# Kernel optimization log

Measured on AMD Instinct MI355X. Metric: run time of the kernel, lower is better.

## Reference

```python
import jax, jax.numpy as jnp
import numpy as np

N_NODES = 10000
N_EDGES = 100000
IN_CH = 384
PROJ = 768  # in_channels * projection_factor
N_BLOCKS = 4
OUT_CH = 128
LN_EPS = 1e-5


def _p(key, shape, fan_in):
    return jax.random.normal(key, shape, dtype=jnp.float32) * (1.0 / np.sqrt(fan_in))


def setup_inputs() -> dict:
    key = jax.random.key(0)
    ks = iter(jax.random.split(key, 64))
    x = jax.random.normal(next(ks), (N_NODES, IN_CH), dtype=jnp.float32)
    edge_index = jax.random.randint(next(ks), (2, N_EDGES), 0, N_NODES, dtype=jnp.int64)
    inp = {
        'x': x,
        'edge_index': edge_index,
        'proj_W': _p(next(ks), (PROJ, IN_CH), IN_CH),
        'proj_b': jnp.zeros((PROJ,), jnp.float32),
        'norm_w': jnp.ones((N_BLOCKS, PROJ), jnp.float32),
        'norm_b': jnp.zeros((N_BLOCKS, PROJ), jnp.float32),
        'g1_W': _p(next(ks), (N_BLOCKS, 4 * 192, PROJ), PROJ),
        'g1_as': _p(next(ks), (N_BLOCKS, 4, 192), 192),
        'g1_ad': _p(next(ks), (N_BLOCKS, 4, 192), 192),
        'g1_b': jnp.zeros((N_BLOCKS, 4 * 192), jnp.float32),
        'g2_W': _p(next(ks), (N_BLOCKS, 2 * 96, PROJ), PROJ),
        'g2_as': _p(next(ks), (N_BLOCKS, 2, 96), 96),
        'g2_ad': _p(next(ks), (N_BLOCKS, 2, 96), 96),
        'g2_b': jnp.zeros((N_BLOCKS, 2 * 96), jnp.float32),
        'uni_W': _p(next(ks), (N_BLOCKS, PROJ, 960), 960),
        'uni_b': jnp.zeros((N_BLOCKS, PROJ), jnp.float32),
        'fnorm_w': jnp.ones((PROJ,), jnp.float32),
        'fnorm_b': jnp.zeros((PROJ,), jnp.float32),
        'fg_W': _p(next(ks), (8 * OUT_CH, PROJ), PROJ),
        'fg_as': _p(next(ks), (8, OUT_CH), OUT_CH),
        'fg_ad': _p(next(ks), (8, OUT_CH), OUT_CH),
        'fg_b': jnp.zeros((OUT_CH,), jnp.float32),
    }
    return inp


def layer_norm(x, w, b):
    m = x.mean(-1, keepdims=True)
    v = ((x - m) ** 2).mean(-1, keepdims=True)
    return (x - m) / jnp.sqrt(v + LN_EPS) * w + b


def gat_conv(x, src, dst, W, a_src, a_dst, bias, heads, out_ch, concat):
    # PyG GATConv (eval mode, add_self_loops already applied in src/dst).
    n = x.shape[0]
    h = (x @ W.T).reshape(n, heads, out_ch)          # [N,H,C]
    al_s = jnp.einsum('nhc,hc->nh', h, a_src)        # [N,H]
    al_d = jnp.einsum('nhc,hc->nh', h, a_dst)
    e = jax.nn.leaky_relu(al_s[src] + al_d[dst], 0.2)  # [E,H]
    emax = jax.ops.segment_max(e, dst, num_segments=n)
    ee = jnp.exp(e - emax[dst])
    den = jax.ops.segment_sum(ee, dst, num_segments=n)
    alpha = ee / (den[dst] + 1e-16)                  # softmax over incoming edges
    out = jax.ops.segment_sum(h[src] * alpha[:, :, None], dst, num_segments=n)
    out = out.reshape(n, heads * out_ch) if concat else out.mean(axis=1)
    return out + bias


def reference(x, edge_index, proj_W, proj_b, norm_w, norm_b,
              g1_W, g1_as, g1_ad, g1_b, g2_W, g2_as, g2_ad, g2_b,
              uni_W, uni_b, fnorm_w, fnorm_b, fg_W, fg_as, fg_ad, fg_b):
    n = x.shape[0]
    loop = jnp.arange(n, dtype=edge_index.dtype)
    src = jnp.concatenate([edge_index[0], loop])  # add self loops (PyG default)
    dst = jnp.concatenate([edge_index[1], loop])

    h = jax.nn.elu(x @ proj_W.T + proj_b)
    for i in range(N_BLOCKS):
        res = h
        hn = layer_norm(h, norm_w[i], norm_b[i])
        o1 = gat_conv(hn, src, dst, g1_W[i], g1_as[i], g1_ad[i], g1_b[i], 4, 192, True)
        o2 = gat_conv(hn, src, dst, g2_W[i], g2_as[i], g2_ad[i], g2_b[i], 2, 96, True)
        cat = jax.nn.elu(jnp.concatenate([o1, o2], axis=-1))  # [N,960]
        h = jax.nn.elu(res + cat @ uni_W[i].T + uni_b[i])
    h = layer_norm(h, fnorm_w, fnorm_b)
    return gat_conv(h, src, dst, fg_W, fg_as, fg_ad, fg_b, 8, OUT_CH, False)
```

## Files before the change

kernel.cpp:

```cpp
#include <hip/hip_runtime.h>
#include <math.h>

#define N_NODES 10000
#define N_EDGES 100000
#define E_TOT   (N_EDGES + N_NODES)
#define PROJ    768
#define LN_EPS  1e-5f

typedef __attribute__((ext_vector_type(8))) short bf16x8;
typedef __attribute__((ext_vector_type(4))) short bf16x4;
typedef __attribute__((ext_vector_type(4))) float f32x4;

__device__ __forceinline__ float elu_f(float x){ return x > 0.f ? x : __expf(x) - 1.f; }
__device__ __forceinline__ float bf2f(unsigned short u){ return __uint_as_float(((unsigned int)u) << 16); }
__device__ __forceinline__ unsigned short f2bf(float f){
  unsigned int u = __float_as_uint(f);
  return (unsigned short)((u + 0x7FFFu + ((u >> 16) & 1u)) >> 16);
}

#define GLOAD16(gp, lp) __builtin_amdgcn_global_load_lds((const __attribute__((address_space(1))) void*)(gp), (__attribute__((address_space(3))) void*)(lp), 16, 0, 0)

__global__ void k_count(const int* __restrict__ ei, int* __restrict__ cnt){
  int e = blockIdx.x*blockDim.x + threadIdx.x;
  if (e >= E_TOT) return;
  int dst = (e < N_EDGES) ? ei[N_EDGES + e] : (e - N_EDGES);
  atomicAdd(&cnt[dst], 1);
}

__global__ void k_scan(const int* __restrict__ cnt, int* __restrict__ indptr, int* __restrict__ pos){
  __shared__ int s[1024];
  __shared__ int s_running;
  int t = threadIdx.x;
  if (t == 0) s_running = 0;
  __syncthreads();
  for (int base = 0; base < N_NODES; base += 1024){
    int v = (base + t < N_NODES) ? cnt[base + t] : 0;
    s[t] = v; __syncthreads();
    for (int off = 1; off < 1024; off <<= 1){
      int add = (t >= off) ? s[t - off] : 0;
      __syncthreads();
      s[t] += add;
      __syncthreads();
    }
    int total = s[1023];
    int run = s_running;
    if (base + t < N_NODES){
      int val = run + s[t] - v;
      indptr[base + t] = val;
      pos[base + t] = val;
    }
    __syncthreads();
    if (t == 0) s_running = run + total;
    __syncthreads();
  }
  if (t == 0) indptr[N_NODES] = s_running;
}

__global__ void k_fill(const int* __restrict__ ei, int* __restrict__ pos,
                       int* __restrict__ csr_src){
  int e = blockIdx.x*blockDim.x + threadIdx.x;
  if (e >= E_TOT) return;
  int s, d;
  if (e < N_EDGES){ s = ei[e]; d = ei[N_EDGES + e]; }
  else            { s = d = e - N_EDGES; }
  int p = atomicAdd(&pos[d], 1);
  csr_src[p] = s;
}

__global__ void k_f2bf_arr4(const float4* __restrict__ in, ushort4* __restrict__ out, int n4){
  int i = blockIdx.x*blockDim.x + threadIdx.x;
  if (i < n4){
    float4 v = in[i];
    ushort4 o;
    o.x = f2bf(v.x); o.y = f2bf(v.y); o.z = f2bf(v.z); o.w = f2bf(v.w);
    out[i] = o;
  }
}

__global__ void k_pack_l1l2(const float* __restrict__ g1, const float* __restrict__ g2,
                            unsigned short* __restrict__ dst){
  int i = blockIdx.x*blockDim.x + threadIdx.x;
  if (i >= 737280) return;
  int layer = i / 184320;
  int off4  = i - layer*184320;
  float4 v;
  if (off4 < 147456) v = *((const float4*)(g1 + (size_t)layer*589824) + off4);
  else               v = *((const float4*)(g2 + (size_t)layer*147456) + (off4 - 147456));
  ushort4 o;
  o.x = f2bf(v.x); o.y = f2bf(v.y); o.z = f2bf(v.z); o.w = f2bf(v.w);
  ((ushort4*)(dst + (size_t)layer*737280))[off4] = o;
}

__global__ void k_layernorm_bf(const unsigned short* __restrict__ x, const float* __restrict__ w,
                               const float* __restrict__ b, unsigned short* __restrict__ y){
  int n = blockIdx.x;
  int t = threadIdx.x;
  const unsigned short* xr = x + (size_t)n*PROJ;
  float v0=0.f, v1=0.f, v2=0.f, v3=0.f;
  if (t < 192){
    bf16x4 hv = *(const bf16x4*)(xr + t*4);
    v0 = bf2f((unsigned short)hv.x); v1 = bf2f((unsigned short)hv.y);
    v2 = bf2f((unsigned short)hv.z); v3 = bf2f((unsigned short)hv.w);
  }
  float s  = v0+v1+v2+v3;
  float s2 = v0*v0 + v1*v1 + v2*v2 + v3*v3;
  #pragma unroll
  for (int off = 32; off; off >>= 1){ s += __shfl_down(s, off); s2 += __shfl_down(s2, off); }
  __shared__ float rs[4], rs2[4];
  __shared__ float s_mean, s_rstd;
  int wid = t >> 6, lane = t & 63;
  if (lane == 0){ rs[wid] = s; rs2[wid] = s2; }
  __syncthreads();
  if (t == 0){
    float S  = rs[0]+rs[1]+rs[2]+rs[3];
    float S2 = rs2[0]+rs2[1]+rs2[2]+rs2[3];
    float m  = S * (1.f/768.f);
    float var = S2 * (1.f/768.f) - m*m;
    s_mean = m; s_rstd = rsqrtf(var + LN_EPS);
  }
  __syncthreads();
  if (t < 192){
    float m = s_mean, r = s_rstd;
    float4 wv = *(const float4*)&w[t*4];
    float4 bv = *(const float4*)&b[t*4];
    ushort4 o;
    o.x = f2bf((v0-m)*r*wv.x + bv.x);
    o.y = f2bf((v1-m)*r*wv.y + bv.y);
    o.z = f2bf((v2-m)*r*wv.z + bv.z);
    o.w = f2bf((v3-m)*r*wv.w + bv.w);
    *(ushort4*)(y + (size_t)n*PROJ + t*4) = o;
  }
}

template<int EPI>
__global__ __launch_bounds__(256, 8)
void k_gemm_mfma(const unsigned short* __restrict__ A, int lda,
                 const unsigned short* __restrict__ W,
                 unsigned short* __restrict__ C, int ldc,
                 int M, int N, int K,
                 const float* __restrict__ bias,
                 const unsigned short* __restrict__ res, int ldres, int NBN){
  __shared__ unsigned short As[2][128*32];
  __shared__ unsigned short Bs[2][64*32];
  const int tid = threadIdx.x;
  const int lane = tid & 63, wid = tid >> 6;
  const int wm = wid >> 1, wn = wid & 1;

  const int nwg = gridDim.x;
  const int q = nwg >> 3, r = nwg & 7;
  const int xcd = blockIdx.x & 7, o = blockIdx.x >> 3;
  const int swz = (xcd < r ? xcd*(q+1) : r*(q+1) + (xcd - r)*q) + o;
  const int bm = (swz / NBN) * 128;
  const int bn = (swz % NBN) * 64;

  const int srow = tid >> 2;
  const int sc   = (tid & 3) ^ ((tid >> 3) & 3);
  size_t ga0 = (size_t)min(bm + srow,      M-1)*lda + sc*8;
  size_t ga1 = (size_t)min(bm + 64 + srow, M-1)*lda + sc*8;
  size_t gb0 = (size_t)min(bn + srow,      N-1)*K   + sc*8;
  const int ldst = tid*8;

  f32x4 acc[4][2];
  #pragma unroll
  for (int i=0;i<4;i++)
    #pragma unroll
    for (int j=0;j<2;j++) acc[i][j] = (f32x4){0.f,0.f,0.f,0.f};

  const int rA = wm*64 + (lane & 15);
  const int rB = wn*32 + (lane & 15);
  const int cu = (((lane >> 4)) ^ (((lane & 15) >> 1) & 3)) * 8;

  const int NT = K >> 5;
  int cur = 0;
  GLOAD16(A + ga0, &As[0][ldst]);
  GLOAD16(A + ga1, &As[0][2048 + ldst]);
  GLOAD16(W + gb0, &Bs[0][ldst]);

  for (int t = 0; t < NT; ++t){
    if (t + 1 < NT){
      const int k0 = (t+1) << 5;
      GLOAD16(A + ga0 + k0, &As[cur^1][ldst]);
      GLOAD16(A + ga1 + k0, &As[cur^1][2048 + ldst]);
      GLOAD16(W + gb0 + k0, &Bs[cur^1][ldst]);
      asm volatile("s_waitcnt vmcnt(3)" ::: "memory");
    } else {
      asm volatile("s_waitcnt vmcnt(0)" ::: "memory");
    }
    __builtin_amdgcn_sched_barrier(0);
    __builtin_amdgcn_s_barrier();
    __builtin_amdgcn_sched_barrier(0);

    bf16x8 af[4], bfr[2];
    #pragma unroll
    for (int mi = 0; mi < 4; mi++)
      af[mi] = *(const bf16x8*)&As[cur][(rA + mi*16)*32 + cu];
    #pragma unroll
    for (int ni = 0; ni < 2; ni++)
      bfr[ni] = *(const bf16x8*)&Bs[cur][(rB + ni*16)*32 + cu];
    #pragma unroll
    for (int mi = 0; mi < 4; mi++)
      #pragma unroll
      for (int ni = 0; ni < 2; ni++)
        acc[mi][ni] = __builtin_amdgcn_mfma_f32_16x16x32_bf16(af[mi], bfr[ni], acc[mi][ni], 0,0,0);

    asm volatile("s_waitcnt lgkmcnt(0)" ::: "memory");
    __builtin_amdgcn_sched_barrier(0);
    __builtin_amdgcn_s_barrier();
    __builtin_amdgcn_sched_barrier(0);
    cur ^= 1;
  }

  const int mrow0 = bm + wm*64 + ((lane>>4)<<2);
  const int ncol0 = bn + wn*32 + (lane & 15);
  #pragma unroll
  for (int mi=0; mi<4; mi++){
    #pragma unroll
    for (int rr=0; rr<4; rr++){
      int m = mrow0 + mi*16 + rr;
      if (m >= M) continue;
      #pragma unroll
      for (int ni=0; ni<2; ni++){
        int n = ncol0 + ni*16;
        float v = acc[mi][ni][rr];
        if (EPI == 1){
          v = elu_f(v + bias[n]);
        } else if (EPI == 2){
          v = elu_f(v + bias[n] + bf2f(res[(size_t)m*ldres + n]));
        }
        C[(size_t)m*ldc + n] = f2bf(v);
      }
    }
  }
}

__global__ void k_attn_coef6(const unsigned short* __restrict__ hlin,
                             const float* __restrict__ as1, const float* __restrict__ ad1,
                             const float* __restrict__ as2, const float* __restrict__ ad2,
                             float* __restrict__ als, float* __restrict__ ald){
  int n = blockIdx.x;
  int wid = threadIdx.x >> 6, lane = threadIdx.x & 63;
  int C    = wid < 4 ? 192 : 96;
  int base = wid < 4 ? wid*192 : 768 + (wid-4)*96;
  const float* as_ = wid < 4 ? as1 + wid*192 : as2 + (wid-4)*96;
  const float* ad_ = wid < 4 ? ad1 + wid*192 : ad2 + (wid-4)*96;
  float ss = 0.f, sd = 0.f;
  if (lane*4 < C){
    bf16x4 hv = *(const bf16x4*)(hlin + (size_t)n*960 + base + lane*4);
    float4 a1 = *(const float4*)&as_[lane*4];
    float4 a2 = *(const float4*)&ad_[lane*4];
    float h0 = bf2f((unsigned short)hv.x), h1 = bf2f((unsigned short)hv.y);
    float h2 = bf2f((unsigned short)hv.z), h3 = bf2f((unsigned short)hv.w);
    ss = h0*a1.x + h1*a1.y + h2*a1.z + h3*a1.w;
    sd = h0*a2.x + h1*a2.y + h2*a2.z + h3*a2.w;
  }
  #pragma unroll
  for (int off = 32; off; off >>= 1){ ss += __shfl_down(ss, off); sd += __shfl_down(sd, off); }
  if (lane == 0){ als[n*6 + wid] = ss; ald[n*6 + wid] = sd; }
}

__global__ void k_attn_coef8(const unsigned short* __restrict__ hlin,
                             const float* __restrict__ a_src, const float* __restrict__ a_dst,
                             float* __restrict__ als, float* __restrict__ ald){
  int n = blockIdx.x;
  int wid = threadIdx.x >> 6, lane = threadIdx.x & 63;
  float ss = 0.f, sd = 0.f;
  if (lane < 32){
    bf16x4 hv = *(const bf16x4*)(hlin + (size_t)n*1024 + wid*128 + lane*4);
    float4 a1 = *(const float4*)&a_src[wid*128 + lane*4];
    float4 a2 = *(const float4*)&a_dst[wid*128 + lane*4];
    float h0 = bf2f((unsigned short)hv.x), h1 = bf2f((unsigned short)hv.y);
    float h2 = bf2f((unsigned short)hv.z), h3 = bf2f((unsigned short)hv.w);
    ss = h0*a1.x + h1*a1.y + h2*a1.z + h3*a1.w;
    sd = h0*a2.x + h1*a2.y + h2*a2.z + h3*a2.w;
  }
  #pragma unroll
  for (int off = 32; off; off >>= 1){ ss += __shfl_down(ss, off); sd += __shfl_down(sd, off); }
  if (lane == 0){ als[n*8 + wid] = ss; ald[n*8 + wid] = sd; }
}

template<int MODE>
__global__ __launch_bounds__(256)
void k_attn_fused(const unsigned short* __restrict__ hlin, int ldh,
                  const float* __restrict__ als, const float* __restrict__ ald,
                  const int* __restrict__ indptr, const int* __restrict__ csr_src,
                  const float* __restrict__ b1, const float* __restrict__ b2,
                  void* __restrict__ outv, int ldo){
  constexpr int TOT = MODE ? 1024 : 960;
  constexpr int HT  = MODE ? 8 : 6;
  constexpr int CH8 = TOT/8;
  constexpr int CPL = (CH8 + 63)/64;
  int n = blockIdx.x;
  int tid = threadIdx.x;
  int wv = tid >> 6, lane = tid & 63;
  int beg = indptr[n], end = indptr[n+1], deg = end - beg;

  __shared__ float s_m[HT], s_dinv[HT], s_ald[HT];
  __shared__ float s_alpha[64*HT];
  __shared__ int   s_src[64];
  __shared__ float s_red[4][TOT];

  for (int h = wv; h < HT; h += 4){
    float aldv = ald[n*HT + h];
    float m = -1e30f, d = 0.f;
    for (int e = beg + lane; e < end; e += 64){
      int s = csr_src[e];
      float v = als[s*HT + h] + aldv;
      v = v > 0.f ? v : 0.2f*v;
      if (v > m){ d *= __expf(m - v); m = v; }
      d += __expf(v - m);
    }
    #pragma unroll
    for (int off = 1; off < 64; off <<= 1){
      float mo_ = __shfl_xor(m, off);
      float dd  = __shfl_xor(d, off);
      float mn  = fmaxf(m, mo_);
      d = d*__expf(m - mn) + dd*__expf(mo_ - mn);
      m = mn;
    }
    if (lane == 0){ s_m[h] = m; s_dinv[h] = 1.f/(d + 1e-16f); s_ald[h] = aldv; }
  }

  int hof[CPL];
  #pragma unroll
  for (int p = 0; p < CPL; p++){
    int idx = (lane + p*64)*8;
    hof[p] = MODE ? (idx >> 7) : (idx < 768 ? idx/192 : 4 + (idx-768)/96);
  }

  f32x4 accA[CPL], accB[CPL];
  #pragma unroll
  for (int p = 0; p < CPL; p++){ accA[p] = (f32x4){0,0,0,0}; accB[p] = (f32x4){0,0,0,0}; }

  for (int base = 0; base < deg; base += 64){
    int chunk = min(64, deg - base);
    __syncthreads();
    if (tid < chunk) s_src[tid] = csr_src[beg + base + tid];
    __syncthreads();
    for (int i = tid; i < chunk*HT; i += 256){
      int e = i / HT, h = i - e*HT;
      float v = als[s_src[e]*HT + h] + s_ald[h];
      v = v > 0.f ? v : 0.2f*v;
      s_alpha[e*HT + h] = __expf(v - s_m[h]) * s_dinv[h];
    }
    __syncthreads();
    for (int e = wv; e < chunk; e += 4){
      int s = s_src[e];
      const bf16x8* hr = (const bf16x8*)(hlin + (size_t)s*ldh);
      const float* ae = &s_alpha[e*HT];
      #pragma unroll
      for (int p = 0; p < CPL; p++){
        int ch = lane + p*64;
        if (CH8 % 64 == 0 || ch < CH8){
          float al = ae[hof[p]];
          bf16x8 hv = hr[ch];
          accA[p].x += bf2f((unsigned short)hv[0])*al;
          accA[p].y += bf2f((unsigned short)hv[1])*al;
          accA[p].z += bf2f((unsigned short)hv[2])*al;
          accA[p].w += bf2f((unsigned short)hv[3])*al;
          accB[p].x += bf2f((unsigned short)hv[4])*al;
          accB[p].y += bf2f((unsigned short)hv[5])*al;
          accB[p].z += bf2f((unsigned short)hv[6])*al;
          accB[p].w += bf2f((unsigned short)hv[7])*al;
        }
      }
    }
  }

  #pragma unroll
  for (int p = 0; p < CPL; p++){
    int ch = lane + p*64;
    if (CH8 % 64 == 0 || ch < CH8){
      *(f32x4*)&s_red[wv][ch*8]     = accA[p];
      *(f32x4*)&s_red[wv][ch*8 + 4] = accB[p];
    }
  }
  __syncthreads();

  if (MODE == 0){
    unsigned short* out = (unsigned short*)outv;
    #pragma unroll
    for (int qq = 0; qq < 4; qq++){
      int idx = tid + qq*256;
      if (idx < TOT){
        float bb = idx < 768 ? b1[idx] : b2[idx - 768];
        float v = s_red[0][idx] + s_red[1][idx] + s_red[2][idx] + s_red[3][idx] + bb;
        out[(size_t)n*ldo + idx] = f2bf(elu_f(v));
      }
    }
  } else {
    float* out = (float*)outv;
    if (tid < 128){
      float v = 0.f;
      #pragma unroll
      for (int h = 0; h < 8; h++){
        int idx = h*128 + tid;
        v += s_red[0][idx] + s_red[1][idx] + s_red[2][idx] + s_red[3][idx];
      }
      out[(size_t)n*ldo + tid] = v*0.125f + b1[tid];
    }
  }
}

extern "C" void kernel_launch(void* const* d_in, const int* in_sizes, int n_in,
                              void* d_out, int out_size, void* d_ws, size_t ws_size,
                              hipStream_t stream){
  const float* x      = (const float*)d_in[0];
  const int*   ei     = (const int*)  d_in[1];
  const float* proj_W = (const float*)d_in[2];
  const float* proj_b = (const float*)d_in[3];
  const float* norm_w = (const float*)d_in[4];
  const float* norm_b = (const float*)d_in[5];
  const float* g1_W   = (const float*)d_in[6];
  const float* g1_as  = (const float*)d_in[7];
  const float* g1_ad  = (const float*)d_in[8];
  const float* g1_b   = (const float*)d_in[9];
  const float* g2_W   = (const float*)d_in[10];
  const float* g2_as  = (const float*)d_in[11];
  const float* g2_ad  = (const float*)d_in[12];
  const float* g2_b   = (const float*)d_in[13];
  const float* uni_W  = (const float*)d_in[14];
  const float* uni_b  = (const float*)d_in[15];
  const float* fnorm_w= (const float*)d_in[16];
  const float* fnorm_b= (const float*)d_in[17];
  const float* fg_W   = (const float*)d_in[18];
  const float* fg_as  = (const float*)d_in[19];
  const float* fg_ad  = (const float*)d_in[20];
  const float* fg_b   = (const float*)d_in[21];

  float* w = (float*)d_ws;
  unsigned short* h  = (unsigned short*)w; w += 3840000;
  unsigned short* h2 = (unsigned short*)w; w += 3840000;
  unsigned short* linbuf = (unsigned short*)w; w += 5120000;
  unsigned short* hnb  = (unsigned short*)w; w += 3840000;
  unsigned short* catb = (unsigned short*)w; w += 4800000;
  unsigned short* wb   = (unsigned short*)w; w += 3489792;
  float* als   = w; w += 80000;
  float* ald   = w; w += 80000;
  int* iw = (int*)w;
  int* cnt     = iw; iw += 10016;
  int* indptr  = iw; iw += 10016;
  int* pos     = iw; iw += 10016;
  int* csr_src = iw; iw += 110016;

  unsigned short* wb_proj = wb;
  unsigned short* wb_l12  = wb_proj + 294912;
  unsigned short* wb_uni  = wb_l12 + 2949120;
  unsigned short* wb_fg   = wb_uni + 2949120;

  hipMemsetAsync(cnt, 0, N_NODES*sizeof(int), stream);
  k_count<<<(E_TOT+255)/256, 256, 0, stream>>>(ei, cnt);
  k_scan<<<1, 1024, 0, stream>>>(cnt, indptr, pos);
  k_fill<<<(E_TOT+255)/256, 256, 0, stream>>>(ei, pos, csr_src);

  k_f2bf_arr4<<<(960000+255)/256, 256, 0, stream>>>((const float4*)x, (ushort4*)hnb, 960000);
  k_f2bf_arr4<<<(73728+255)/256,  256, 0, stream>>>((const float4*)proj_W, (ushort4*)wb_proj, 73728);
  k_pack_l1l2<<<(737280+255)/256, 256, 0, stream>>>(g1_W, g2_W, wb_l12);
  k_f2bf_arr4<<<(737280+255)/256, 256, 0, stream>>>((const float4*)uni_W, (ushort4*)wb_uni, 737280);
  k_f2bf_arr4<<<(196608+255)/256, 256, 0, stream>>>((const float4*)fg_W, (ushort4*)wb_fg, 196608);

  dim3 blk(256);

  k_gemm_mfma<1><<<dim3(79*12), blk, 0, stream>>>(hnb, 384, wb_proj, h, 768, N_NODES, 768, 384, proj_b, nullptr, 0, 12);

  unsigned short* cur = h;
  unsigned short* oth = h2;
  for (int i = 0; i < 4; i++){
    k_layernorm_bf<<<N_NODES, 256, 0, stream>>>(cur, norm_w + i*768, norm_b + i*768, hnb);
    k_gemm_mfma<0><<<dim3(79*15), blk, 0, stream>>>(hnb, 768, wb_l12 + (size_t)i*737280, linbuf, 960, N_NODES, 960, 768, nullptr, nullptr, 0, 15);
    k_attn_coef6<<<N_NODES, 384, 0, stream>>>(linbuf, g1_as + i*768, g1_ad + i*768, g2_as + i*192, g2_ad + i*192, als, ald);
    k_attn_fused<0><<<N_NODES, 256, 0, stream>>>(linbuf, 960, als, ald, indptr, csr_src, g1_b + i*768, g2_b + i*192, catb, 960);
    k_gemm_mfma<2><<<dim3(79*12), blk, 0, stream>>>(catb, 960, wb_uni + (size_t)i*737280, oth, 768, N_NODES, 768, 960, uni_b + i*768, cur, 768, 12);
    unsigned short* t = cur; cur = oth; oth = t;
  }

  k_layernorm_bf<<<N_NODES, 256, 0, stream>>>(cur, fnorm_w, fnorm_b, hnb);
  k_gemm_mfma<0><<<dim3(79*16), blk, 0, stream>>>(hnb, 768, wb_fg, linbuf, 1024, N_NODES, 1024, 768, nullptr, nullptr, 0, 16);
  k_attn_coef8<<<N_NODES, 512, 0, stream>>>(linbuf, fg_as, fg_ad, als, ald);
  k_attn_fused<1><<<N_NODES, 256, 0, stream>>>(linbuf, 1024, als, ald, indptr, csr_src, fg_b, nullptr, d_out, 128);
}
```

Before: 696.4 us.

## Triple-buffer GEMM LDS, unroll attention aggregation, merge bf16 conversion launches

The MFMA GEMM moves from a double to a triple LDS buffer ring. This lets it drop the second barrier and lgkmcnt wait per k-step, since the buffer being written is never the one still being read. The attention aggregation loop now handles two edges per wave iteration, issuing both row loads before the FMAs to add memory-level parallelism. Four fp32-to-bf16 conversion launches are merged into one multi-segment kernel to cut launch overhead. The tradeoff is more LDS per block, which may lower occupancy, plus extra registers in the attention kernel.

```diff
diff --git a/kernel.cpp b/kernel.cpp
--- a/kernel.cpp
+++ b/kernel.cpp
@@ -67,14 +67,21 @@
   csr_src[p] = s;
 }
 
-__global__ void k_f2bf_arr4(const float4* __restrict__ in, ushort4* __restrict__ out, int n4){
+__global__ void k_f2bf_multi(const float4* __restrict__ s0, ushort4* __restrict__ d0, int n0,
+                             const float4* __restrict__ s1, ushort4* __restrict__ d1, int n1,
+                             const float4* __restrict__ s2, ushort4* __restrict__ d2, int n2,
+                             const float4* __restrict__ s3, ushort4* __restrict__ d3, int n3){
   int i = blockIdx.x*blockDim.x + threadIdx.x;
-  if (i < n4){
-    float4 v = in[i];
-    ushort4 o;
-    o.x = f2bf(v.x); o.y = f2bf(v.y); o.z = f2bf(v.z); o.w = f2bf(v.w);
-    out[i] = o;
-  }
+  const float4* src; ushort4* dst; int idx;
+  if (i < n0){ src = s0; dst = d0; idx = i; }
+  else if (i < n0+n1){ src = s1; dst = d1; idx = i-n0; }
+  else if (i < n0+n1+n2){ src = s2; dst = d2; idx = i-n0-n1; }
+  else if (i < n0+n1+n2+n3){ src = s3; dst = d3; idx = i-n0-n1-n2; }
+  else return;
+  float4 v = src[idx];
+  ushort4 o;
+  o.x = f2bf(v.x); o.y = f2bf(v.y); o.z = f2bf(v.z); o.w = f2bf(v.w);
+  dst[idx] = o;
 }
 
 __global__ void k_pack_l1l2(const float* __restrict__ g1, const float* __restrict__ g2,
@@ -140,8 +147,8 @@
                  int M, int N, int K,
                  const float* __restrict__ bias,
                  const unsigned short* __restrict__ res, int ldres, int NBN){
-  __shared__ unsigned short As[2][128*32];
-  __shared__ unsigned short Bs[2][64*32];
+  __shared__ unsigned short As[3][128*32];
+  __shared__ unsigned short Bs[3][64*32];
   const int tid = threadIdx.x;
   const int lane = tid & 63, wid = tid >> 6;
   const int wm = wid >> 1, wn = wid & 1;
@@ -171,17 +178,18 @@
   const int cu = (((lane >> 4)) ^ (((lane & 15) >> 1) & 3)) * 8;
 
   const int NT = K >> 5;
-  int cur = 0;
+  int bcur = 0;
   GLOAD16(A + ga0, &As[0][ldst]);
   GLOAD16(A + ga1, &As[0][2048 + ldst]);
   GLOAD16(W + gb0, &Bs[0][ldst]);
 
   for (int t = 0; t < NT; ++t){
     if (t + 1 < NT){
+      int bst = bcur + 1; if (bst == 3) bst = 0;
       const int k0 = (t+1) << 5;
-      GLOAD16(A + ga0 + k0, &As[cur^1][ldst]);
-      GLOAD16(A + ga1 + k0, &As[cur^1][2048 + ldst]);
-      GLOAD16(W + gb0 + k0, &Bs[cur^1][ldst]);
+      GLOAD16(A + ga0 + k0, &As[bst][ldst]);
+      GLOAD16(A + ga1 + k0, &As[bst][2048 + ldst]);
+      GLOAD16(W + gb0 + k0, &Bs[bst][ldst]);
       asm volatile("s_waitcnt vmcnt(3)" ::: "memory");
     } else {
       asm volatile("s_waitcnt vmcnt(0)" ::: "memory");
@@ -193,21 +201,17 @@
     bf16x8 af[4], bfr[2];
     #pragma unroll
     for (int mi = 0; mi < 4; mi++)
-      af[mi] = *(const bf16x8*)&As[cur][(rA + mi*16)*32 + cu];
+      af[mi] = *(const bf16x8*)&As[bcur][(rA + mi*16)*32 + cu];
     #pragma unroll
     for (int ni = 0; ni < 2; ni++)
-      bfr[ni] = *(const bf16x8*)&Bs[cur][(rB + ni*16)*32 + cu];
+      bfr[ni] = *(const bf16x8*)&Bs[bcur][(rB + ni*16)*32 + cu];
     #pragma unroll
     for (int mi = 0; mi < 4; mi++)
       #pragma unroll
       for (int ni = 0; ni < 2; ni++)
         acc[mi][ni] = __builtin_amdgcn_mfma_f32_16x16x32_bf16(af[mi], bfr[ni], acc[mi][ni], 0,0,0);
 
-    asm volatile("s_waitcnt lgkmcnt(0)" ::: "memory");
-    __builtin_amdgcn_sched_barrier(0);
-    __builtin_amdgcn_s_barrier();
-    __builtin_amdgcn_sched_barrier(0);
-    cur ^= 1;
+    bcur += 1; if (bcur == 3) bcur = 0;
   }
 
   const int mrow0 = bm + wm*64 + ((lane>>4)<<2);
@@ -343,7 +347,37 @@
       s_alpha[e*HT + h] = __expf(v - s_m[h]) * s_dinv[h];
     }
     __syncthreads();
-    for (int e = wv; e < chunk; e += 4){
+
+    int e = wv;
+    for (; e + 4 < chunk; e += 8){
+      int s0 = s_src[e], s1 = s_src[e+4];
+      const bf16x8* hr0 = (const bf16x8*)(hlin + (size_t)s0*ldh);
+      const bf16x8* hr1 = (const bf16x8*)(hlin + (size_t)s1*ldh);
+      const float* ae0 = &s_alpha[e*HT];
+      const float* ae1 = &s_alpha[(e+4)*HT];
+      bf16x8 hv0[CPL], hv1[CPL];
+      #pragma unroll
+      for (int p = 0; p < CPL; p++){
+        int ch = lane + p*64;
+        if (CH8 % 64 == 0 || ch < CH8){ hv0[p] = hr0[ch]; hv1[p] = hr1[ch]; }
+      }
+      #pragma unroll
+      for (int p = 0; p < CPL; p++){
+        int ch = lane + p*64;
+        if (CH8 % 64 == 0 || ch < CH8){
+          float a0 = ae0[hof[p]], a1 = ae1[hof[p]];
+          accA[p].x += bf2f((unsigned short)hv0[p][0])*a0 + bf2f((unsigned short)hv1[p][0])*a1;
+          accA[p].y += bf2f((unsigned short)hv0[p][1])*a0 + bf2f((unsigned short)hv1[p][1])*a1;
+          accA[p].z += bf2f((unsigned short)hv0[p][2])*a0 + bf2f((unsigned short)hv1[p][2])*a1;
+          accA[p].w += bf2f((unsigned short)hv0[p][3])*a0 + bf2f((unsigned short)hv1[p][3])*a1;
+          accB[p].x += bf2f((unsigned short)hv0[p][4])*a0 + bf2f((unsigned short)hv1[p][4])*a1;
+          accB[p].y += bf2f((unsigned short)hv0[p][5])*a0 + bf2f((unsigned short)hv1[p][5])*a1;
+          accB[p].z += bf2f((unsigned short)hv0[p][6])*a0 + bf2f((unsigned short)hv1[p][6])*a1;
+          accB[p].w += bf2f((unsigned short)hv0[p][7])*a0 + bf2f((unsigned short)hv1[p][7])*a1;
+        }
+      }
+    }
+    for (; e < chunk; e += 4){
       int s = s_src[e];
       const bf16x8* hr = (const bf16x8*)(hlin + (size_t)s*ldh);
       const float* ae = &s_alpha[e*HT];
@@ -452,11 +486,12 @@
   k_scan<<<1, 1024, 0, stream>>>(cnt, indptr, pos);
   k_fill<<<(E_TOT+255)/256, 256, 0, stream>>>(ei, pos, csr_src);
 
-  k_f2bf_arr4<<<(960000+255)/256, 256, 0, stream>>>((const float4*)x, (ushort4*)hnb, 960000);
-  k_f2bf_arr4<<<(73728+255)/256,  256, 0, stream>>>((const float4*)proj_W, (ushort4*)wb_proj, 73728);
+  k_f2bf_multi<<<(1967616+255)/256, 256, 0, stream>>>(
+      (const float4*)x, (ushort4*)hnb, 960000,
+      (const float4*)proj_W, (ushort4*)wb_proj, 73728,
+      (const float4*)uni_W, (ushort4*)wb_uni, 737280,
+      (const float4*)fg_W, (ushort4*)wb_fg, 196608);
   k_pack_l1l2<<<(737280+255)/256, 256, 0, stream>>>(g1_W, g2_W, wb_l12);
-  k_f2bf_arr4<<<(737280+255)/256, 256, 0, stream>>>((const float4*)uni_W, (ushort4*)wb_uni, 737280);
-  k_f2bf_arr4<<<(196608+255)/256, 256, 0, stream>>>((const float4*)fg_W, (ushort4*)wb_fg, 196608);
 
   dim3 blk(256);
 
```

Result: no change. 699.0 us (+0.4%).
